# Performance work log

Measured on AMD Instinct MI355X. Metric: run time of the kernel, lower is better.

Reference implementation:

```python
import jax, jax.numpy as jnp
import numpy as np

Q, G, H, K, C, O = 20000, 20000, 32, 15, 128, 128


def setup_inputs() -> dict:
    key = jax.random.key(0)
    k1, k2, k3, k4, k5, k6 = jax.random.split(key, 6)
    return {
        "query_points": jax.random.normal(k1, (Q, 3), dtype=jnp.float32),
        "support_points": jax.random.normal(k2, (G, 3), dtype=jnp.float32),
        "support_features": jax.random.normal(k3, (G, C), dtype=jnp.float32),
        "kernel": jax.random.normal(k4, (K, 3), dtype=jnp.float32),
        "weights": jax.random.normal(k5, (K, C, O), dtype=jnp.float32),
        # KDTree KNN indices are precomputed int constants; random in-range
        # indices give identical math/perf characteristics.
        "neighbor_indices": jax.random.randint(k6, (Q, H), 0, G, dtype=jnp.int32),
    }


def reference(query_points, support_points, support_features, kernel, weights, neighbor_indices):
    # Faithful to original: neighbor_points gathered from query_points
    # (original code indexes query_points, not support_points; requires Q == G).
    neighbor_points = query_points[neighbor_indices]          # [Q, H, 3]
    neighbor_features = support_features[neighbor_indices]    # [Q, H, C]
    # diff: [Q, H, K, 3] = neighbor - query - kernel_point
    diff = neighbor_points[:, :, None, :] - query_points[:, None, None, :] - kernel
    distances = jnp.sqrt(jnp.sum(diff * diff, axis=-1))        # [Q, H, K]
    sigma = 1.0
    influences = jax.nn.relu(1.0 - distances / sigma)          # [Q, H, K]
    # 3-way contraction over h, k, c  -> [Q, O]
    result = jnp.einsum("qhk,kco,qhc->qo", influences, weights, neighbor_features)
    return result
```

## Files before the change

### kernel.cpp

```cpp
#include <hip/hip_runtime.h>
#include <hip/hip_bf16.h>


typedef short bf16x8 __attribute__((ext_vector_type(8)));
typedef float f32x4 __attribute__((ext_vector_type(4)));

constexpr int Qn = 20000;
constexpr int Hn = 32;
constexpr int Kn = 15;
constexpr int Cn = 128;
constexpr int On = 128;
constexpr int QB = 16;
constexpr int BLOCK = 512;

constexpr int F_OFF     = 0;
constexpr int NPT_OFF   = 0;
constexpr int DENSE_OFF = 8192;
constexpr int NIDX_OFF  = 24576;
constexpr int HLIST_OFF = 26624;
constexpr int QPL_OFF   = 27648;
constexpr int KPL_OFF   = 27904;
constexpr int FLG_OFF   = 28160;
constexpr int INFL_OFF  = 32768;
constexpr int GLIST_OFF = 49152;
constexpr int CNT_OFF   = 51200;
constexpr int POOL_SZ   = 51264;

__device__ __forceinline__ unsigned short bfu(float x) {
  union { __hip_bfloat16 h; unsigned short s; } cv;
  cv.h = __float2bfloat16(x);
  return cv.s;
}
__device__ __forceinline__ unsigned pk2(float a, float b) {
  union { __hip_bfloat162 h2; unsigned u; } cv;
  cv.h2 = __float22bfloat162_rn(make_float2(a, b));
  return cv.u;
}

__global__ void conv_w(const float* __restrict__ wts, unsigned* __restrict__ wfrag) {
  int tid = blockIdx.x * 256 + threadIdx.x;
  int wsel = tid & 3;
  int l    = (tid >> 2) & 63;
  int kt   = (tid >> 8) & 63;
  int nt   = tid >> 14;
  int col  = nt * 16 + (l & 15);
  int ck   = kt * 32 + (l >> 4) * 8 + wsel * 2;
  int k0 = ck & 15, c0 = ck >> 4;
  int k1 = k0 + 1;
  float a = wts[(k0 * Cn + c0) * On + col];
  float b = (k1 < Kn) ? wts[(k1 * Cn + c0) * On + col] : 0.f;
  wfrag[tid] = pk2(a, b);
}

__global__ __launch_bounds__(BLOCK, 4)
void kpconv_main(const float* __restrict__ qpts,
                 const float* __restrict__ sfeat,
                 const float* __restrict__ kpts,
                 const int* __restrict__ nidx,
                 const unsigned* __restrict__ wfrag,
                 float* __restrict__ out) {
  __shared__ __align__(16) char pool[POOL_SZ];
  const int t = threadIdx.x;
  const int qbase = blockIdx.x * QB;
  const int l = t & 63, w = t >> 6;
  const int lg = l >> 4, li = l & 15;

  {
    *(unsigned*)(pool + GLIST_OFF + t * 4) = 0u;
    int g = nidx[(size_t)qbase * Hn + t];
    *(int*)(pool + NIDX_OFF + t * 4) = g;
    float* np = (float*)(pool + NPT_OFF + t * 16);
    np[0] = qpts[g * 3 + 0];
    np[1] = qpts[g * 3 + 1];
    np[2] = qpts[g * 3 + 2];
    if (t < 16) {
      *(unsigned*)(pool + FLG_OFF + t * 4) = 0u;
      float* qp = (float*)(pool + QPL_OFF + t * 16);
      qp[0] = qpts[(qbase + t) * 3 + 0];
      qp[1] = qpts[(qbase + t) * 3 + 1];
      qp[2] = qpts[(qbase + t) * 3 + 2];
    }
    if (t >= 32 && t < 32 + Kn) {
      int k = t - 32;
      float* kp = (float*)(pool + KPL_OFF + k * 16);
      kp[0] = kpts[k * 3 + 0];
      kp[1] = kpts[k * 3 + 1];
      kp[2] = kpts[k * 3 + 2];
    }
  }
  __syncthreads();

#pragma unroll
  for (int it = 0; it < 16; ++it) {
    int idx = t + it * BLOCK;
    int k = idx & 15, h = (idx >> 4) & 31, q = idx >> 9;
    unsigned short v = 0;
    if (k < Kn) {
      const float* np = (const float*)(pool + NPT_OFF + (q * 32 + h) * 16);
      const float* qp = (const float*)(pool + QPL_OFF + q * 16);
      const float* kp = (const float*)(pool + KPL_OFF + k * 16);
      float dx = np[0] - qp[0] - kp[0];
      float dy = np[1] - qp[1] - kp[1];
      float dz = np[2] - qp[2] - kp[2];
      float d = sqrtf(dx * dx + dy * dy + dz * dz);
      float inf = fmaxf(0.f, 1.f - d);
      if (inf > 0.f) atomicOr((unsigned*)(pool + FLG_OFF) + q, 1u << h);
      v = bfu(inf);
    }
    *(unsigned short*)(pool + DENSE_OFF + q * 1024 + h * 32 + k * 2) = v;
  }
  __syncthreads();

  if (t < 16) {
    unsigned m = *(unsigned*)(pool + FLG_OFF + t * 4);
    *(int*)(pool + CNT_OFF + t * 4) = __popc(m);
    int i = 0;
    while (m) {
      int h = __ffs(m) - 1; m &= m - 1;
      *(short*)(pool + HLIST_OFF + t * 64 + i * 2) = (short)h;
      *(int*)(pool + GLIST_OFF + t * 128 + i * 4) =
          *(const int*)(pool + NIDX_OFF + (t * 32 + h) * 4);
      ++i;
    }
  }
  __syncthreads();

#pragma unroll
  for (int it = 0; it < 16; ++it) {
    int idx = t + it * BLOCK;
    int slot = idx & 31, k = (idx >> 5) & 15, q = idx >> 9;
    int cnt = *(const int*)(pool + CNT_OFF + q * 4);
    unsigned short v = 0;
    if (k < Kn && slot < cnt) {
      int h = *(const short*)(pool + HLIST_OFF + q * 64 + slot * 2);
      v = *(const unsigned short*)(pool + DENSE_OFF + q * 1024 + h * 32 + k * 2);
    }
    unsigned byte = (unsigned)(q * 1024) +
        (((unsigned)(k * 64 + slot * 2)) ^ (((unsigned)k & 7u) << 4));
    *(unsigned short*)(pool + INFL_OFF + byte) = v;
  }
  __syncthreads();

  const int ctl = w & 3, qg = w >> 2;
  const unsigned abase0 = (unsigned)INFL_OFF +
      (((unsigned)(li * 64 + lg * 16)) ^ (((unsigned)li & 7u) << 4));
  const int cl = ctl * 16 + li;
  const unsigned wswz = ((unsigned)cl & 7u) << 4;
  const unsigned wbase0 = (unsigned)((cl >> 1) * 1024 +
                                     ((cl & 1) * 2 + (lg >> 1)) * 256 +
                                     (lg & 1) * 8);
  const unsigned liB = (unsigned)(lg * 256 + li * 16);
  const unsigned sLg = ((unsigned)(lg >> 1)) << 4;
  const uint4* wfp = (const uint4*)wfrag + (size_t)w * 4096 + l;
  f32x4 acc0 = {0.f, 0.f, 0.f, 0.f}, acc1 = {0.f, 0.f, 0.f, 0.f};

#pragma unroll 1
  for (int r = 0; r < 2; ++r) {
    const int cbase = r * 64 + cl;
#pragma unroll 2
    for (int qi = 0; qi < 8; ++qi) {
      const int q = qg * 8 + qi;
      int cnt = *(const int*)(pool + CNT_OFF + q * 4);
      bf16x8 afrag = *(const bf16x8*)(pool + abase0 + q * 1024);
      uint4 ga = *(const uint4*)(pool + GLIST_OFF + q * 128 + lg * 32);
      uint4 gb = *(const uint4*)(pool + GLIST_OFF + q * 128 + lg * 32 + 16);
      int s0 = lg * 8;
      float v0 = (s0 + 0 < cnt) ? sfeat[(size_t)ga.x * Cn + cbase] : 0.f;
      float v1 = (s0 + 1 < cnt) ? sfeat[(size_t)ga.y * Cn + cbase] : 0.f;
      float v2 = (s0 + 2 < cnt) ? sfeat[(size_t)ga.z * Cn + cbase] : 0.f;
      float v3 = (s0 + 3 < cnt) ? sfeat[(size_t)ga.w * Cn + cbase] : 0.f;
      float v4 = (s0 + 4 < cnt) ? sfeat[(size_t)gb.x * Cn + cbase] : 0.f;
      float v5 = (s0 + 5 < cnt) ? sfeat[(size_t)gb.y * Cn + cbase] : 0.f;
      float v6 = (s0 + 6 < cnt) ? sfeat[(size_t)gb.z * Cn + cbase] : 0.f;
      float v7 = (s0 + 7 < cnt) ? sfeat[(size_t)gb.w * Cn + cbase] : 0.f;
      uint4 bu;
      bu.x = pk2(v0, v1); bu.y = pk2(v2, v3);
      bu.z = pk2(v4, v5); bu.w = pk2(v6, v7);
      bf16x8 bfrag = *(bf16x8*)&bu;
      f32x4 z = {0.f, 0.f, 0.f, 0.f};
      f32x4 d = __builtin_amdgcn_mfma_f32_16x16x32_bf16(afrag, bfrag, z, 0, 0, 0);
      unsigned byte = (wbase0 + (unsigned)(q * 16)) ^ wswz;
      *(uint2*)(pool + byte) = make_uint2(pk2(d[0], d[1]), pk2(d[2], d[3]));
    }
    __syncthreads();

    const int ktbase = r * 32;
#pragma unroll
    for (int kt = 0; kt < 32; kt += 2) {
      unsigned a0 = ((unsigned)(kt << 10) + liB) ^ (sLg | (((unsigned)kt & 3u) << 5));
      unsigned a1 = ((unsigned)((kt + 1) << 10) + liB) ^ (sLg | (((unsigned)(kt + 1) & 3u) << 5));
      bf16x8 f0 = *(const bf16x8*)(pool + a0);
      uint4 w0 = wfp[(size_t)(ktbase + kt) * 64];
      bf16x8 f1 = *(const bf16x8*)(pool + a1);
      uint4 w1 = wfp[(size_t)(ktbase + kt + 1) * 64];
      acc0 = __builtin_amdgcn_mfma_f32_16x16x32_bf16(f0, *(bf16x8*)&w0, acc0, 0, 0, 0);
      acc1 = __builtin_amdgcn_mfma_f32_16x16x32_bf16(f1, *(bf16x8*)&w1, acc1, 0, 0, 0);
    }
    __syncthreads();
  }

  {
    f32x4 acc = acc0 + acc1;
    float* ob = out + (size_t)qbase * On + w * 16 + li;
#pragma unroll
    for (int rr = 0; rr < 4; ++rr)
      ob[(lg * 4 + rr) * On] = acc[rr];
  }
}

extern "C" void kernel_launch(void* const* d_in, const int* in_sizes, int n_in,
                              void* d_out, int out_size, void* d_ws, size_t ws_size,
                              hipStream_t stream) {
  const float* qpts  = (const float*)d_in[0];
  const float* sfeat = (const float*)d_in[2];
  const float* kpts  = (const float*)d_in[3];
  const float* wts   = (const float*)d_in[4];
  const int*   nidx  = (const int*)d_in[5];
  float* outp = (float*)d_out;
  unsigned* wfrag = (unsigned*)d_ws;

  conv_w<<<512, 256, 0, stream>>>(wts, wfrag);
  kpconv_main<<<Qn / QB, BLOCK, 0, stream>>>(qpts, sfeat, kpts, nidx, wfrag, outp);
}
```

Measured before the change: 233.0 us.

## Pack neighbor indices into spare influence row and gather all channels in one pass

Each query's active neighbor indices are now stored as 16-bit values in the unused k=15 row of the swizzled influence tile, with a sentinel marking empty slots. This replaces the separate gather list and the per-query count check. The feature-gather/MFMA stage now covers all 128 channels in one pass using a 64 KB LDS buffer, followed by a single 64-step weight contraction. That removes the two-round loop and its extra barriers. In exchange, shared memory per block rises from about 51 KB to 80 KB, which can reduce how many blocks fit on a CU. The k=15 row stays harmless in the contraction only because its weights are zero and the packed index bits decode as finite bf16 values.

```diff
diff --git a/kernel.cpp b/kernel.cpp
--- a/kernel.cpp
+++ b/kernel.cpp
@@ -11,9 +11,13 @@
 constexpr int Cn = 128;
 constexpr int On = 128;
 constexpr int QB = 16;
+constexpr int KT = 64;
 constexpr int BLOCK = 512;
+constexpr unsigned SENT = 20000u;
 
 constexpr int F_OFF     = 0;
+constexpr int INFL_OFF  = 65536;
+constexpr int POOL_SZ   = 81920;
 constexpr int NPT_OFF   = 0;
 constexpr int DENSE_OFF = 8192;
 constexpr int NIDX_OFF  = 24576;
@@ -21,10 +25,7 @@
 constexpr int QPL_OFF   = 27648;
 constexpr int KPL_OFF   = 27904;
 constexpr int FLG_OFF   = 28160;
-constexpr int INFL_OFF  = 32768;
-constexpr int GLIST_OFF = 49152;
-constexpr int CNT_OFF   = 51200;
-constexpr int POOL_SZ   = 51264;
+constexpr int CNT_OFF   = 28224;
 
 __device__ __forceinline__ unsigned short bfu(float x) {
   union { __hip_bfloat16 h; unsigned short s; } cv;
@@ -66,7 +67,6 @@
   const int lg = l >> 4, li = l & 15;
 
   {
-    *(unsigned*)(pool + GLIST_OFF + t * 4) = 0u;
     int g = nidx[(size_t)qbase * Hn + t];
     *(int*)(pool + NIDX_OFF + t * 4) = g;
     float* np = (float*)(pool + NPT_OFF + t * 16);
@@ -118,8 +118,6 @@
     while (m) {
       int h = __ffs(m) - 1; m &= m - 1;
       *(short*)(pool + HLIST_OFF + t * 64 + i * 2) = (short)h;
-      *(int*)(pool + GLIST_OFF + t * 128 + i * 4) =
-          *(const int*)(pool + NIDX_OFF + (t * 32 + h) * 4);
       ++i;
     }
   }
@@ -130,10 +128,19 @@
     int idx = t + it * BLOCK;
     int slot = idx & 31, k = (idx >> 5) & 15, q = idx >> 9;
     int cnt = *(const int*)(pool + CNT_OFF + q * 4);
-    unsigned short v = 0;
-    if (k < Kn && slot < cnt) {
-      int h = *(const short*)(pool + HLIST_OFF + q * 64 + slot * 2);
-      v = *(const unsigned short*)(pool + DENSE_OFF + q * 1024 + h * 32 + k * 2);
+    unsigned short v;
+    if (k == 15) {
+      v = (unsigned short)SENT;
+      if (slot < cnt) {
+        int h = *(const short*)(pool + HLIST_OFF + q * 64 + slot * 2);
+        v = (unsigned short)(*(const int*)(pool + NIDX_OFF + (q * 32 + h) * 4));
+      }
+    } else {
+      v = 0;
+      if (slot < cnt) {
+        int h = *(const short*)(pool + HLIST_OFF + q * 64 + slot * 2);
+        v = *(const unsigned short*)(pool + DENSE_OFF + q * 1024 + h * 32 + k * 2);
+      }
     }
     unsigned byte = (unsigned)(q * 1024) +
         (((unsigned)(k * 64 + slot * 2)) ^ (((unsigned)k & 7u) << 4));
@@ -141,38 +148,32 @@
   }
   __syncthreads();
 
-  const int ctl = w & 3, qg = w >> 2;
-  const unsigned abase0 = (unsigned)INFL_OFF +
-      (((unsigned)(li * 64 + lg * 16)) ^ (((unsigned)li & 7u) << 4));
-  const int cl = ctl * 16 + li;
-  const unsigned wswz = ((unsigned)cl & 7u) << 4;
-  const unsigned wbase0 = (unsigned)((cl >> 1) * 1024 +
-                                     ((cl & 1) * 2 + (lg >> 1)) * 256 +
-                                     (lg & 1) * 8);
-  const unsigned liB = (unsigned)(lg * 256 + li * 16);
-  const unsigned sLg = ((unsigned)(lg >> 1)) << 4;
-  const uint4* wfp = (const uint4*)wfrag + (size_t)w * 4096 + l;
-  f32x4 acc0 = {0.f, 0.f, 0.f, 0.f}, acc1 = {0.f, 0.f, 0.f, 0.f};
-
-#pragma unroll 1
-  for (int r = 0; r < 2; ++r) {
-    const int cbase = r * 64 + cl;
+  {
+    const int c = w * 16 + li;
+    const unsigned abase0 = (unsigned)INFL_OFF +
+        (((unsigned)(li * 64 + lg * 16)) ^ (((unsigned)li & 7u) << 4));
+    const unsigned glof = (unsigned)INFL_OFF +
+        (((unsigned)(15 * 64 + lg * 16)) ^ 0x70u);
+    const unsigned wswz = ((unsigned)c & 7u) << 4;
+    const unsigned wbase0 = (unsigned)((c >> 1) * 1024 +
+                                       ((c & 1) * 2 + (lg >> 1)) * 256 +
+                                       (lg & 1) * 8);
 #pragma unroll 2
-    for (int qi = 0; qi < 8; ++qi) {
-      const int q = qg * 8 + qi;
-      int cnt = *(const int*)(pool + CNT_OFF + q * 4);
+    for (int q = 0; q < QB; ++q) {
       bf16x8 afrag = *(const bf16x8*)(pool + abase0 + q * 1024);
-      uint4 ga = *(const uint4*)(pool + GLIST_OFF + q * 128 + lg * 32);
-      uint4 gb = *(const uint4*)(pool + GLIST_OFF + q * 128 + lg * 32 + 16);
-      int s0 = lg * 8;
-      float v0 = (s0 + 0 < cnt) ? sfeat[(size_t)ga.x * Cn + cbase] : 0.f;
-      float v1 = (s0 + 1 < cnt) ? sfeat[(size_t)ga.y * Cn + cbase] : 0.f;
-      float v2 = (s0 + 2 < cnt) ? sfeat[(size_t)ga.z * Cn + cbase] : 0.f;
-      float v3 = (s0 + 3 < cnt) ? sfeat[(size_t)ga.w * Cn + cbase] : 0.f;
-      float v4 = (s0 + 4 < cnt) ? sfeat[(size_t)gb.x * Cn + cbase] : 0.f;
-      float v5 = (s0 + 5 < cnt) ? sfeat[(size_t)gb.y * Cn + cbase] : 0.f;
-      float v6 = (s0 + 6 < cnt) ? sfeat[(size_t)gb.z * Cn + cbase] : 0.f;
-      float v7 = (s0 + 7 < cnt) ? sfeat[(size_t)gb.w * Cn + cbase] : 0.f;
+      uint4 gl = *(const uint4*)(pool + glof + q * 1024);
+      unsigned g0 = gl.x & 0xFFFFu, g1 = gl.x >> 16;
+      unsigned g2 = gl.y & 0xFFFFu, g3 = gl.y >> 16;
+      unsigned g4 = gl.z & 0xFFFFu, g5 = gl.z >> 16;
+      unsigned g6 = gl.w & 0xFFFFu, g7 = gl.w >> 16;
+      float v0 = (g0 < SENT) ? sfeat[(size_t)g0 * Cn + c] : 0.f;
+      float v1 = (g1 < SENT) ? sfeat[(size_t)g1 * Cn + c] : 0.f;
+      float v2 = (g2 < SENT) ? sfeat[(size_t)g2 * Cn + c] : 0.f;
+      float v3 = (g3 < SENT) ? sfeat[(size_t)g3 * Cn + c] : 0.f;
+      float v4 = (g4 < SENT) ? sfeat[(size_t)g4 * Cn + c] : 0.f;
+      float v5 = (g5 < SENT) ? sfeat[(size_t)g5 * Cn + c] : 0.f;
+      float v6 = (g6 < SENT) ? sfeat[(size_t)g6 * Cn + c] : 0.f;
+      float v7 = (g7 < SENT) ? sfeat[(size_t)g7 * Cn + c] : 0.f;
       uint4 bu;
       bu.x = pk2(v0, v1); bu.y = pk2(v2, v3);
       bu.z = pk2(v4, v5); bu.w = pk2(v6, v7);
@@ -182,24 +183,25 @@
       unsigned byte = (wbase0 + (unsigned)(q * 16)) ^ wswz;
       *(uint2*)(pool + byte) = make_uint2(pk2(d[0], d[1]), pk2(d[2], d[3]));
     }
-    __syncthreads();
-
-    const int ktbase = r * 32;
-#pragma unroll
-    for (int kt = 0; kt < 32; kt += 2) {
+  }
+  __syncthreads();
+
+  {
+    const unsigned liB = (unsigned)(lg * 256 + li * 16);
+    const unsigned sLg = ((unsigned)(lg >> 1)) << 4;
+    const uint4* wfp = (const uint4*)wfrag + (size_t)w * 4096 + l;
+    f32x4 acc0 = {0.f, 0.f, 0.f, 0.f}, acc1 = {0.f, 0.f, 0.f, 0.f};
+#pragma unroll 8
+    for (int kt = 0; kt < KT; kt += 2) {
       unsigned a0 = ((unsigned)(kt << 10) + liB) ^ (sLg | (((unsigned)kt & 3u) << 5));
       unsigned a1 = ((unsigned)((kt + 1) << 10) + liB) ^ (sLg | (((unsigned)(kt + 1) & 3u) << 5));
       bf16x8 f0 = *(const bf16x8*)(pool + a0);
-      uint4 w0 = wfp[(size_t)(ktbase + kt) * 64];
+      uint4 w0 = wfp[(size_t)kt * 64];
       bf16x8 f1 = *(const bf16x8*)(pool + a1);
-      uint4 w1 = wfp[(size_t)(ktbase + kt + 1) * 64];
+      uint4 w1 = wfp[(size_t)(kt + 1) * 64];
       acc0 = __builtin_amdgcn_mfma_f32_16x16x32_bf16(f0, *(bf16x8*)&w0, acc0, 0, 0, 0);
       acc1 = __builtin_amdgcn_mfma_f32_16x16x32_bf16(f1, *(bf16x8*)&w1, acc1, 0, 0, 0);
     }
-    __syncthreads();
-  }
-
-  {
     f32x4 acc = acc0 + acc1;
     float* ob = out + (size_t)qbase * On + w * 16 + li;
 #pragma unroll
```

Measured after the change: 223.8 us. -3.9%, faster.
